# Optimization experiments

Measured on AMD Instinct MI355X. Metric: run time of the kernel, lower is better.

Reference implementation:

```python
import jax, jax.numpy as jnp
import numpy as np

B, C, N = 4, 256, 2048
H = 8
HD = C // H  # head_dim = 32


def setup_inputs() -> dict:
    key = jax.random.key(0)
    ks = jax.random.split(key, 5)
    s = 1.0 / np.sqrt(C)
    return {
        "x": jax.random.normal(ks[0], (B, C, 3, N), dtype=jnp.float32),
        "Wq": jax.random.normal(ks[1], (C, C), dtype=jnp.float32) * s,
        "Wk": jax.random.normal(ks[2], (C, C), dtype=jnp.float32) * s,
        "Wv": jax.random.normal(ks[3], (C, C), dtype=jnp.float32) * s,
        "Wo": jax.random.normal(ks[4], (C, C), dtype=jnp.float32) * s,
    }


def _vn_linear(W, x):
    # nn.Linear over channel axis: out[b,o,d,n] = sum_c W[o,c] x[b,c,d,n]
    return jnp.einsum('oc,bcdn->bodn', W, x)


def _heads(t):
    # [B,C,3,N] -> [B,H,N,HD,3]
    return t.reshape(B, H, HD, 3, N).transpose(0, 1, 4, 2, 3)


def reference(x, Wq, Wk, Wv, Wo):
    q = _heads(_vn_linear(Wq, x))
    k = _heads(_vn_linear(Wk, x))
    v = _heads(_vn_linear(Wv, x))
    # energy contracts over (head_dim, 3)
    energy = jnp.einsum('bhnci,bhmci->bhnm', q, k)
    attn = jax.nn.softmax(energy / np.sqrt(HD), axis=-1)
    out = jnp.einsum('bhnm,bhmci->bhnci', attn, v)
    # [B,H,N,HD,3] -> [B,C,3,N]
    out = out.transpose(0, 1, 3, 4, 2).reshape(B, C, 3, N)
    out = _vn_linear(Wo, out)
    return out + x
```

## Files before the change

kernel.cpp:

```cpp
#include <hip/hip_runtime.h>
#include <hip/hip_bf16.h>
#include <cmath>


typedef unsigned short u16;
typedef unsigned int   u32;
typedef u16   u16x8  __attribute__((ext_vector_type(8)));
typedef short s16x8  __attribute__((ext_vector_type(8)));
typedef float f32x4  __attribute__((ext_vector_type(4)));
typedef float f32x16 __attribute__((ext_vector_type(16)));

namespace {
constexpr int Nc = 2048, Fc = 96;
constexpr float SCALE_LOG2 = 0.17677669529663687f * 1.4426950408889634f;
constexpr float DEFER_THR  = 8.0f;
constexpr int KP = 104;
constexpr int VP = 72;
constexpr int VOFF = 64 * KP;
constexpr int SBUF = VOFF + 96 * VP;
}

__device__ inline float fast_exp2(float x) {
#if __has_builtin(__builtin_amdgcn_exp2f)
    return __builtin_amdgcn_exp2f(x);
#else
    return exp2f(x);
#endif
}

__device__ inline u16 f2bf(float x) {
    union { float f; unsigned u; } v; v.f = x;
    unsigned r = v.u + 0x7FFFu + ((v.u >> 16) & 1u);
    return (u16)(r >> 16);
}

__global__ __launch_bounds__(256) void wconv_kernel(
    const float* __restrict__ Wq, const float* __restrict__ Wk,
    const float* __restrict__ Wv, const float* __restrict__ Wo,
    u16* __restrict__ Wb)
{
    const int id = blockIdx.x * 256 + threadIdx.x;
    const int base = id * 8;
    const int o = base >> 8, c = base & 255;
    const int sel = o >> 8, ol = o & 255;
    const float* src = (sel == 0) ? Wq : (sel == 1) ? Wk : (sel == 2) ? Wv : Wo;
    const float sc = (sel == 0) ? SCALE_LOG2 : 1.0f;
    const float4 a = *(const float4*)&src[(size_t)ol * 256 + c];
    const float4 b = *(const float4*)&src[(size_t)ol * 256 + c + 4];
    u16x8 r;
    r[0]=f2bf(a.x*sc); r[1]=f2bf(a.y*sc); r[2]=f2bf(a.z*sc); r[3]=f2bf(a.w*sc);
    r[4]=f2bf(b.x*sc); r[5]=f2bf(b.y*sc); r[6]=f2bf(b.z*sc); r[7]=f2bf(b.w*sc);
    *(u16x8*)&Wb[(size_t)o * 256 + c] = r;
}

__global__ __launch_bounds__(256) void xt_kernel(
    const float* __restrict__ x, u16* __restrict__ xt)
{
    const int nt = blockIdx.x, ct = blockIdx.y, bi = blockIdx.z;
    const int b = bi / 3, i = bi % 3;
    const int t = (int)threadIdx.x;
    const int n0 = nt * 64, c0 = ct * 64;

    __shared__ u16 tile[64][72];

    const int n_l = t & 63;
#pragma unroll
    for (int it = 0; it < 16; ++it) {
        const int c_l = (t >> 6) + it * 4;
        tile[n_l][c_l] =
            f2bf(x[(((size_t)(b * 256 + c0 + c_l)) * 3 + i) * Nc + n0 + n_l]);
    }
    __syncthreads();
#pragma unroll
    for (int it = 0; it < 2; ++it) {
        const int idx = t + it * 256;
        const int nn = idx >> 3, part = idx & 7;
        *(u16x8*)&xt[((size_t)bi * Nc + n0 + nn) * 256 + c0 + part * 8] =
            *(const u16x8*)&tile[nn][part * 8];
    }
}

__global__ __launch_bounds__(256) void qkv_gemm_kernel(
    const u16* __restrict__ xt, const u16* __restrict__ wb,
    u16* __restrict__ Qt, u16* __restrict__ Kt, u16* __restrict__ Vf)
{
    const int nt = blockIdx.x;
    const int wy = blockIdx.y;
    const int bi = blockIdx.z;
    const int b = bi / 3, i = bi % 3;
    const int wsel = wy >> 1, ot = wy & 1;

    const u16* xs = xt + ((size_t)bi * Nc + nt * 128) * 256;
    const u16* ws = wb + (size_t)(wsel * 256 + ot * 128) * 256;

    __shared__ u16 xl[128][40];
    __shared__ u16 wl[128][40];

    const int t = (int)threadIdx.x;
    const int wv = t >> 6, lane = t & 63;
    const int g = lane >> 4, c16 = lane & 15;
    const int wr = wv >> 1, wc = wv & 1;

    f32x4 acc[4][4];
#pragma unroll
    for (int mi = 0; mi < 4; ++mi)
#pragma unroll
        for (int ni = 0; ni < 4; ++ni)
#pragma unroll
            for (int r = 0; r < 4; ++r) acc[mi][ni][r] = 0.f;

    for (int ks = 0; ks < 8; ++ks) {
        __syncthreads();
#pragma unroll
        for (int it = 0; it < 2; ++it) {
            const int idx = t + it * 256;
            const int row = idx >> 2, part = idx & 3;
            *(u16x8*)&xl[row][part * 8] =
                *(const u16x8*)&xs[(size_t)row * 256 + ks * 32 + part * 8];
            *(u16x8*)&wl[row][part * 8] =
                *(const u16x8*)&ws[(size_t)row * 256 + ks * 32 + part * 8];
        }
        __syncthreads();

        s16x8 af[4], bf[4];
        if (wsel < 2) {
#pragma unroll
            for (int mi = 0; mi < 4; ++mi) af[mi] = *(const s16x8*)&xl[wr*64 + mi*16 + c16][g*8];
#pragma unroll
            for (int ni = 0; ni < 4; ++ni) bf[ni] = *(const s16x8*)&wl[wc*64 + ni*16 + c16][g*8];
        } else {
#pragma unroll
            for (int mi = 0; mi < 4; ++mi) af[mi] = *(const s16x8*)&wl[wr*64 + mi*16 + c16][g*8];
#pragma unroll
            for (int ni = 0; ni < 4; ++ni) bf[ni] = *(const s16x8*)&xl[wc*64 + ni*16 + c16][g*8];
        }
#pragma unroll
        for (int mi = 0; mi < 4; ++mi)
#pragma unroll
            for (int ni = 0; ni < 4; ++ni)
                acc[mi][ni] = __builtin_amdgcn_mfma_f32_16x16x32_bf16(
                    af[mi], bf[ni], acc[mi][ni], 0, 0, 0);
    }

    if (wsel < 2) {
        u16* dst = wsel ? Kt : Qt;
#pragma unroll
        for (int mi = 0; mi < 4; ++mi)
#pragma unroll
            for (int ni = 0; ni < 4; ++ni) {
                const int o = ot * 128 + wc * 64 + ni * 16 + c16;
                const int h = o >> 5, cw = o & 31;
#pragma unroll
                for (int r = 0; r < 4; ++r) {
                    const int n = nt * 128 + wr * 64 + mi * 16 + g * 4 + r;
                    dst[((size_t)(b * 8 + h) * Nc + n) * Fc + i * 32 + cw] =
                        f2bf(acc[mi][ni][r]);
                }
            }
    } else {
#pragma unroll
        for (int mi = 0; mi < 4; ++mi)
#pragma unroll
            for (int ni = 0; ni < 4; ++ni) {
                const int n = nt * 128 + wc * 64 + ni * 16 + c16;
#pragma unroll
                for (int r = 0; r < 4; ++r) {
                    const int o = ot * 128 + wr * 64 + mi * 16 + g * 4 + r;
                    const int h = o >> 5, cw = o & 31;
                    Vf[((size_t)(b * 8 + h) * Fc + i * 32 + cw) * Nc + n] =
                        f2bf(acc[mi][ni][r]);
                }
            }
    }
}

__global__ __launch_bounds__(256) void attn_mfma_kernel(
    const u16* __restrict__ Qt, const u16* __restrict__ Kt,
    const u16* __restrict__ Vf, u16* __restrict__ aot)
{
    const int bid = (int)blockIdx.x;
    const int lid = (bid & 7) * 64 + (bid >> 3);
    const int bh = lid >> 4;
    const int qt = lid & 15;

    const int t    = (int)threadIdx.x;
    const int wq   = t >> 6;
    const int lane = t & 63;
    const int ql   = lane & 31;
    const int hi   = lane >> 5;

    __shared__ u16 sbuf[2][SBUF];

    const int qb = qt * 128 + wq * 32;

    s16x8 bq[6];
#pragma unroll
    for (int s6 = 0; s6 < 6; ++s6)
        bq[s6] = *(const s16x8*)&Qt[((size_t)bh * Nc + qb + ql) * Fc + s6 * 16 + hi * 8];

    const u16* g_src[6]; int g_str[6], g_dst[6];
#pragma unroll
    for (int it = 0; it < 6; ++it) {
        if (it < 3) {
            const int c = t + it * 256;
            const int row = c / 12, part = c - row * 12;
            g_src[it] = Kt + ((size_t)bh * Nc + row) * Fc + part * 8;
            g_str[it] = 64 * Fc;
            g_dst[it] = row * KP + part * 8;
        } else {
            const int c = t + (it - 3) * 256;
            const int f = c >> 3, part = c & 7;
            g_src[it] = Vf + ((size_t)bh * Fc + f) * Nc + part * 8;
            g_str[it] = 64;
            g_dst[it] = VOFF + f * VP + part * 8;
        }
    }

    f32x16 acc[3];
#pragma unroll
    for (int ft = 0; ft < 3; ++ft)
#pragma unroll
        for (int r = 0; r < 16; ++r) acc[ft][r] = 0.f;
    float m_s = -INFINITY, l_s = 0.f;

    u16x8 sreg[6];
#pragma unroll
    for (int it = 0; it < 6; ++it) sreg[it] = *(const u16x8*)g_src[it];
#pragma unroll
    for (int it = 0; it < 6; ++it) *(u16x8*)&sbuf[0][g_dst[it]] = sreg[it];
#pragma unroll
    for (int it = 0; it < 6; ++it)
        sreg[it] = *(const u16x8*)(g_src[it] + (size_t)g_str[it]);
    __syncthreads();

    for (int kt = 0; kt < 32; ++kt) {
        const int cur = kt & 1;
        if (kt < 31) {
#pragma unroll
            for (int it = 0; it < 6; ++it) *(u16x8*)&sbuf[cur ^ 1][g_dst[it]] = sreg[it];
        }
        if (kt < 30) {
#pragma unroll
            for (int it = 0; it < 6; ++it)
                sreg[it] = *(const u16x8*)(g_src[it] + (size_t)(kt + 2) * g_str[it]);
        }

        const u16* kb = &sbuf[cur][0];
        const u16* vb = &sbuf[cur][VOFF];

        f32x16 sv0, sv1;
#pragma unroll
        for (int r = 0; r < 16; ++r) { sv0[r] = 0.f; sv1[r] = 0.f; }
        __builtin_amdgcn_s_setprio(1);
#pragma unroll
        for (int s6 = 0; s6 < 6; ++s6) {
            const s16x8 ka0 = *(const s16x8*)&kb[ql * KP + s6 * 16 + hi * 8];
            sv0 = __builtin_amdgcn_mfma_f32_32x32x16_bf16(ka0, bq[s6], sv0, 0, 0, 0);
            const s16x8 ka1 = *(const s16x8*)&kb[(32 + ql) * KP + s6 * 16 + hi * 8];
            sv1 = __builtin_amdgcn_mfma_f32_32x32x16_bf16(ka1, bq[s6], sv1, 0, 0, 0);
        }
        __builtin_amdgcn_s_setprio(0);

        float mx[16];
#pragma unroll
        for (int r = 0; r < 16; ++r) mx[r] = fmaxf(sv0[r], sv1[r]);
#pragma unroll
        for (int s = 8; s > 0; s >>= 1)
#pragma unroll
            for (int r = 0; r < 16; ++r) if (r < s) mx[r] = fmaxf(mx[r], mx[r + s]);
        const float mloc = fmaxf(mx[0], __shfl_xor(mx[0], 32));

        if (__any(mloc > m_s + DEFER_THR)) {
            const float mnew = fmaxf(m_s, mloc);
            const float esc = fast_exp2(m_s - mnew);
            m_s = mnew; l_s *= esc;
#pragma unroll
            for (int ft = 0; ft < 3; ++ft)
#pragma unroll
                for (int r = 0; r < 16; ++r) acc[ft][r] *= esc;
        }

#pragma unroll
        for (int r = 0; r < 16; ++r) {
            sv0[r] = fast_exp2(sv0[r] - m_s);
            sv1[r] = fast_exp2(sv1[r] - m_s);
        }
        float ls[16];
#pragma unroll
        for (int r = 0; r < 16; ++r) ls[r] = sv0[r] + sv1[r];
#pragma unroll
        for (int s = 8; s > 0; s >>= 1)
#pragma unroll
            for (int r = 0; r < 16; ++r) if (r < s) ls[r] += ls[r + s];
        l_s += ls[0] + __shfl_xor(ls[0], 32);

        u32 pk0[8], pk1[8];
#pragma unroll
        for (int j = 0; j < 8; ++j) {
            asm("v_cvt_pk_bf16_f32 %0, %1, %2" : "=v"(pk0[j]) : "v"(sv0[2*j]), "v"(sv0[2*j+1]));
            asm("v_cvt_pk_bf16_f32 %0, %1, %2" : "=v"(pk1[j]) : "v"(sv1[2*j]), "v"(sv1[2*j+1]));
        }
        asm volatile("v_permlane32_swap_b32 %0, %1" : "+v"(pk0[0]), "+v"(pk0[2]));
        asm volatile("v_permlane32_swap_b32 %0, %1" : "+v"(pk0[1]), "+v"(pk0[3]));
        asm volatile("v_permlane32_swap_b32 %0, %1" : "+v"(pk0[4]), "+v"(pk0[6]));
        asm volatile("v_permlane32_swap_b32 %0, %1" : "+v"(pk0[5]), "+v"(pk0[7]));
        asm volatile("v_permlane32_swap_b32 %0, %1" : "+v"(pk1[0]), "+v"(pk1[2]));
        asm volatile("v_permlane32_swap_b32 %0, %1" : "+v"(pk1[1]), "+v"(pk1[3]));
        asm volatile("v_permlane32_swap_b32 %0, %1" : "+v"(pk1[4]), "+v"(pk1[6]));
        asm volatile("v_permlane32_swap_b32 %0, %1" : "+v"(pk1[5]), "+v"(pk1[7]));
        union U { u32 w[4]; s16x8 v; } pb[4];
        pb[0].w[0]=pk0[0]; pb[0].w[1]=pk0[1]; pb[0].w[2]=pk0[2]; pb[0].w[3]=pk0[3];
        pb[1].w[0]=pk0[4]; pb[1].w[1]=pk0[5]; pb[1].w[2]=pk0[6]; pb[1].w[3]=pk0[7];
        pb[2].w[0]=pk1[0]; pb[2].w[1]=pk1[1]; pb[2].w[2]=pk1[2]; pb[2].w[3]=pk1[3];
        pb[3].w[0]=pk1[4]; pb[3].w[1]=pk1[5]; pb[3].w[2]=pk1[6]; pb[3].w[3]=pk1[7];

        __builtin_amdgcn_s_setprio(1);
#pragma unroll
        for (int ft = 0; ft < 3; ++ft) {
#pragma unroll
            for (int ks = 0; ks < 4; ++ks) {
                const s16x8 va = *(const s16x8*)&vb[(ft * 32 + ql) * VP + ks * 16 + hi * 8];
                acc[ft] = __builtin_amdgcn_mfma_f32_32x32x16_bf16(va, pb[ks].v, acc[ft], 0, 0, 0);
            }
        }
        __builtin_amdgcn_s_setprio(0);

        __syncthreads();
    }

    const float inv = 1.f / l_s;
    u16* ot = &sbuf[0][0] + wq * (32 * 104);
#pragma unroll
    for (int ft = 0; ft < 3; ++ft)
#pragma unroll
        for (int r = 0; r < 16; ++r) {
            const int frow = (r & 3) + 8 * (r >> 2) + 4 * hi;
            ot[ql * 104 + ft * 32 + frow] = f2bf(acc[ft][r] * inv);
        }
    __syncthreads();

    u16x8 v6[6];
#pragma unroll
    for (int j = 0; j < 6; ++j)
        v6[j] = *(const u16x8*)&ot[ql * 104 + hi * 48 + j * 8];

    const int n = qb + ql;
    const int b_ = bh >> 3, h_ = bh & 7;
    const size_t base0 = ((size_t)(b_ * 3 + 0) * Nc + n) * 256 + h_ * 32;
    const size_t base1 = ((size_t)(b_ * 3 + 1) * Nc + n) * 256 + h_ * 32;
    const size_t base2 = ((size_t)(b_ * 3 + 2) * Nc + n) * 256 + h_ * 32;
    if (hi == 0) {
        *(u16x8*)&aot[base0 +  0] = v6[0];
        *(u16x8*)&aot[base0 +  8] = v6[1];
        *(u16x8*)&aot[base0 + 16] = v6[2];
        *(u16x8*)&aot[base0 + 24] = v6[3];
        *(u16x8*)&aot[base1 +  0] = v6[4];
        *(u16x8*)&aot[base1 +  8] = v6[5];
    } else {
        *(u16x8*)&aot[base1 + 16] = v6[0];
        *(u16x8*)&aot[base1 + 24] = v6[1];
        *(u16x8*)&aot[base2 +  0] = v6[2];
        *(u16x8*)&aot[base2 +  8] = v6[3];
        *(u16x8*)&aot[base2 + 16] = v6[4];
        *(u16x8*)&aot[base2 + 24] = v6[5];
    }
}

__global__ __launch_bounds__(256) void out_gemm_kernel(
    const u16* __restrict__ aot, const u16* __restrict__ wb,
    const float* __restrict__ x, float* __restrict__ out)
{
    const int nt = blockIdx.x, ot = blockIdx.y, bi = blockIdx.z;
    const int b = bi / 3, i = bi % 3;

    const u16* bs = aot + ((size_t)bi * Nc + nt * 128) * 256;
    const u16* ws = wb + (size_t)(768 + ot * 128) * 256;

    __shared__ u16 al[128][40];
    __shared__ u16 wl[128][40];

    const int t = (int)threadIdx.x;
    const int wv = t >> 6, lane = t & 63;
    const int g = lane >> 4, c16 = lane & 15;
    const int wr = wv >> 1, wc = wv & 1;

    f32x4 acc[4][4];
#pragma unroll
    for (int mi = 0; mi < 4; ++mi)
#pragma unroll
        for (int ni = 0; ni < 4; ++ni)
#pragma unroll
            for (int r = 0; r < 4; ++r) acc[mi][ni][r] = 0.f;

    for (int ks = 0; ks < 8; ++ks) {
        __syncthreads();
#pragma unroll
        for (int it = 0; it < 2; ++it) {
            const int idx = t + it * 256;
            const int row = idx >> 2, part = idx & 3;
            *(u16x8*)&al[row][part * 8] =
                *(const u16x8*)&bs[(size_t)row * 256 + ks * 32 + part * 8];
            *(u16x8*)&wl[row][part * 8] =
                *(const u16x8*)&ws[(size_t)row * 256 + ks * 32 + part * 8];
        }
        __syncthreads();

        s16x8 af[4], bf[4];
#pragma unroll
        for (int mi = 0; mi < 4; ++mi) af[mi] = *(const s16x8*)&wl[wr*64 + mi*16 + c16][g*8];
#pragma unroll
        for (int ni = 0; ni < 4; ++ni) bf[ni] = *(const s16x8*)&al[wc*64 + ni*16 + c16][g*8];
#pragma unroll
        for (int mi = 0; mi < 4; ++mi)
#pragma unroll
            for (int ni = 0; ni < 4; ++ni)
                acc[mi][ni] = __builtin_amdgcn_mfma_f32_16x16x32_bf16(
                    af[mi], bf[ni], acc[mi][ni], 0, 0, 0);
    }

#pragma unroll
    for (int mi = 0; mi < 4; ++mi)
#pragma unroll
        for (int ni = 0; ni < 4; ++ni) {
            const int n = nt * 128 + wc * 64 + ni * 16 + c16;
#pragma unroll
            for (int r = 0; r < 4; ++r) {
                const int o = ot * 128 + wr * 64 + mi * 16 + g * 4 + r;
                const size_t idx = ((size_t)(b * 256 + o) * 3 + i) * Nc + n;
                out[idx] = x[idx] + acc[mi][ni][r];
            }
        }
}

extern "C" void kernel_launch(void* const* d_in, const int* in_sizes, int n_in,
                              void* d_out, int out_size, void* d_ws, size_t ws_size,
                              hipStream_t stream) {
    const float* x  = (const float*)d_in[0];
    const float* Wq = (const float*)d_in[1];
    const float* Wk = (const float*)d_in[2];
    const float* Wv = (const float*)d_in[3];
    const float* Wo = (const float*)d_in[4];
    float* out = (float*)d_out;

    const size_t E = (size_t)32 * Fc * Nc;
    u16* xt  = (u16*)d_ws;
    u16* wbw = xt + E;
    u16* qt  = wbw + 262144;
    u16* kt  = qt + E;
    u16* vf  = kt + E;
    u16* aot = vf + E;

    dim3 blk(256);
    wconv_kernel    <<<dim3(128),        blk, 0, stream>>>(Wq, Wk, Wv, Wo, wbw);
    xt_kernel       <<<dim3(32, 4, 12),  blk, 0, stream>>>(x, xt);
    qkv_gemm_kernel <<<dim3(16, 6, 12),  blk, 0, stream>>>(xt, wbw, qt, kt, vf);
    attn_mfma_kernel<<<dim3(512),        blk, 0, stream>>>(qt, kt, vf, aot);
    out_gemm_kernel <<<dim3(16, 2, 12),  blk, 0, stream>>>(aot, wbw, x, out);
}
```

Before: 135.6 us.

## Software-pipeline QK^T one tile ahead with triple-buffered 32-key LDS tiles

Shrinks the attention key tile from 64 to 32 keys and triple-buffers K/V tiles in shared memory. The QK^T MFMAs for the next tile are issued before the softmax and PV of the current tile, with two score accumulators swapped alternately. The aim is to overlap the exp/reduction VALU work with matrix-core work and hide LDS loads. The cost is twice as many iterations and barriers, more LDS in use, and extra registers for the second score tile, and the setprio hints are removed.

```diff
diff --git a/kernel.cpp b/kernel.cpp
--- a/kernel.cpp
+++ b/kernel.cpp
@@ -15,8 +15,8 @@
 constexpr float SCALE_LOG2 = 0.17677669529663687f * 1.4426950408889634f;
 constexpr float DEFER_THR  = 8.0f;
 constexpr int KP = 104;
-constexpr int VP = 72;
-constexpr int VOFF = 64 * KP;
+constexpr int VP = 40;
+constexpr int VOFF = 32 * KP;
 constexpr int SBUF = VOFF + 96 * VP;
 }
 
@@ -183,13 +183,13 @@
     const int bh = lid >> 4;
     const int qt = lid & 15;
 
-    const int t    = (int)threadIdx.x;
-    const int wq   = t >> 6;
-    const int lane = t & 63;
+    const int t_   = (int)threadIdx.x;
+    const int wq   = t_ >> 6;
+    const int lane = t_ & 63;
     const int ql   = lane & 31;
     const int hi   = lane >> 5;
 
-    __shared__ u16 sbuf[2][SBUF];
+    __shared__ u16 sbuf[3 * SBUF];
 
     const int qb = qt * 128 + wq * 32;
 
@@ -198,20 +198,19 @@
     for (int s6 = 0; s6 < 6; ++s6)
         bq[s6] = *(const s16x8*)&Qt[((size_t)bh * Nc + qb + ql) * Fc + s6 * 16 + hi * 8];
 
-    const u16* g_src[6]; int g_str[6], g_dst[6];
-#pragma unroll
-    for (int it = 0; it < 6; ++it) {
-        if (it < 3) {
-            const int c = t + it * 256;
+    const u16* g_cur[3]; int g_str[3], g_dst[3];
+#pragma unroll
+    for (int it = 0; it < 3; ++it) {
+        const int c = t_ + it * 256;
+        if (c < 384) {
             const int row = c / 12, part = c - row * 12;
-            g_src[it] = Kt + ((size_t)bh * Nc + row) * Fc + part * 8;
-            g_str[it] = 64 * Fc;
+            g_cur[it] = Kt + ((size_t)bh * Nc + row) * Fc + part * 8;
+            g_str[it] = 32 * Fc;
             g_dst[it] = row * KP + part * 8;
         } else {
-            const int c = t + (it - 3) * 256;
-            const int f = c >> 3, part = c & 7;
-            g_src[it] = Vf + ((size_t)bh * Fc + f) * Nc + part * 8;
-            g_str[it] = 64;
+            const int c2 = c - 384, f = c2 >> 2, part = c2 & 3;
+            g_cur[it] = Vf + ((size_t)bh * Fc + f) * Nc + part * 8;
+            g_str[it] = 32;
             g_dst[it] = VOFF + f * VP + part * 8;
         }
     }
@@ -223,51 +222,61 @@
         for (int r = 0; r < 16; ++r) acc[ft][r] = 0.f;
     float m_s = -INFINITY, l_s = 0.f;
 
-    u16x8 sreg[6];
-#pragma unroll
-    for (int it = 0; it < 6; ++it) sreg[it] = *(const u16x8*)g_src[it];
-#pragma unroll
-    for (int it = 0; it < 6; ++it) *(u16x8*)&sbuf[0][g_dst[it]] = sreg[it];
-#pragma unroll
-    for (int it = 0; it < 6; ++it)
-        sreg[it] = *(const u16x8*)(g_src[it] + (size_t)g_str[it]);
+    u16* b0 = sbuf;
+    u16* b1 = sbuf + SBUF;
+    u16* b2 = sbuf + 2 * SBUF;
+
+    u16x8 sreg[3];
+#pragma unroll
+    for (int it = 0; it < 3; ++it) { sreg[it] = *(const u16x8*)g_cur[it]; g_cur[it] += g_str[it]; }
+#pragma unroll
+    for (int it = 0; it < 3; ++it) *(u16x8*)&b0[g_dst[it]] = sreg[it];
+#pragma unroll
+    for (int it = 0; it < 3; ++it) { sreg[it] = *(const u16x8*)g_cur[it]; g_cur[it] += g_str[it]; }
     __syncthreads();
 
-    for (int kt = 0; kt < 32; ++kt) {
-        const int cur = kt & 1;
-        if (kt < 31) {
-#pragma unroll
-            for (int it = 0; it < 6; ++it) *(u16x8*)&sbuf[cur ^ 1][g_dst[it]] = sreg[it];
-        }
-        if (kt < 30) {
-#pragma unroll
-            for (int it = 0; it < 6; ++it)
-                sreg[it] = *(const u16x8*)(g_src[it] + (size_t)(kt + 2) * g_str[it]);
-        }
-
-        const u16* kb = &sbuf[cur][0];
-        const u16* vb = &sbuf[cur][VOFF];
-
-        f32x16 sv0, sv1;
-#pragma unroll
-        for (int r = 0; r < 16; ++r) { sv0[r] = 0.f; sv1[r] = 0.f; }
-        __builtin_amdgcn_s_setprio(1);
-#pragma unroll
-        for (int s6 = 0; s6 < 6; ++s6) {
-            const s16x8 ka0 = *(const s16x8*)&kb[ql * KP + s6 * 16 + hi * 8];
-            sv0 = __builtin_amdgcn_mfma_f32_32x32x16_bf16(ka0, bq[s6], sv0, 0, 0, 0);
-            const s16x8 ka1 = *(const s16x8*)&kb[(32 + ql) * KP + s6 * 16 + hi * 8];
-            sv1 = __builtin_amdgcn_mfma_f32_32x32x16_bf16(ka1, bq[s6], sv1, 0, 0, 0);
-        }
-        __builtin_amdgcn_s_setprio(0);
-
-        float mx[16];
-#pragma unroll
-        for (int r = 0; r < 16; ++r) mx[r] = fmaxf(sv0[r], sv1[r]);
-#pragma unroll
-        for (int s = 8; s > 0; s >>= 1)
-#pragma unroll
-            for (int r = 0; r < 16; ++r) if (r < s) mx[r] = fmaxf(mx[r], mx[r + s]);
+    f32x16 svE, svO;
+#pragma unroll
+    for (int r = 0; r < 16; ++r) svE[r] = 0.f;
+#pragma unroll
+    for (int s6 = 0; s6 < 6; ++s6) {
+        const s16x8 ka = *(const s16x8*)&b0[ql * KP + s6 * 16 + hi * 8];
+        svE = __builtin_amdgcn_mfma_f32_32x32x16_bf16(ka, bq[s6], svE, 0, 0, 0);
+    }
+#pragma unroll
+    for (int it = 0; it < 3; ++it) *(u16x8*)&b1[g_dst[it]] = sreg[it];
+#pragma unroll
+    for (int it = 0; it < 3; ++it) { sreg[it] = *(const u16x8*)g_cur[it]; g_cur[it] += g_str[it]; }
+    __syncthreads();
+
+    u16 *bA = b0, *bB = b1, *bC = b2;
+
+    auto body = [&](int t, f32x16& SC, f32x16& SN) {
+        if (t < 63) {
+#pragma unroll
+            for (int r = 0; r < 16; ++r) SN[r] = 0.f;
+#pragma unroll
+            for (int s6 = 0; s6 < 6; ++s6) {
+                const s16x8 ka = *(const s16x8*)&bB[ql * KP + s6 * 16 + hi * 8];
+                SN = __builtin_amdgcn_mfma_f32_32x32x16_bf16(ka, bq[s6], SN, 0, 0, 0);
+            }
+        }
+        if (t < 62) {
+#pragma unroll
+            for (int it = 0; it < 3; ++it) *(u16x8*)&bC[g_dst[it]] = sreg[it];
+        }
+        if (t < 61) {
+#pragma unroll
+            for (int it = 0; it < 3; ++it) { sreg[it] = *(const u16x8*)g_cur[it]; g_cur[it] += g_str[it]; }
+        }
+
+        float mx[8];
+#pragma unroll
+        for (int r = 0; r < 8; ++r) mx[r] = fmaxf(SC[r], SC[r + 8]);
+#pragma unroll
+        for (int s = 4; s > 0; s >>= 1)
+#pragma unroll
+            for (int r = 0; r < 8; ++r) if (r < s) mx[r] = fmaxf(mx[r], mx[r + s]);
         const float mloc = fmaxf(mx[0], __shfl_xor(mx[0], 32));
 
         if (__any(mloc > m_s + DEFER_THR)) {
@@ -281,55 +290,49 @@
         }
 
 #pragma unroll
-        for (int r = 0; r < 16; ++r) {
-            sv0[r] = fast_exp2(sv0[r] - m_s);
-            sv1[r] = fast_exp2(sv1[r] - m_s);
-        }
-        float ls[16];
-#pragma unroll
-        for (int r = 0; r < 16; ++r) ls[r] = sv0[r] + sv1[r];
-#pragma unroll
-        for (int s = 8; s > 0; s >>= 1)
-#pragma unroll
-            for (int r = 0; r < 16; ++r) if (r < s) ls[r] += ls[r + s];
+        for (int r = 0; r < 16; ++r) SC[r] = fast_exp2(SC[r] - m_s);
+        float ls[8];
+#pragma unroll
+        for (int r = 0; r < 8; ++r) ls[r] = SC[r] + SC[r + 8];
+#pragma unroll
+        for (int s = 4; s > 0; s >>= 1)
+#pragma unroll
+            for (int r = 0; r < 8; ++r) if (r < s) ls[r] += ls[r + s];
         l_s += ls[0] + __shfl_xor(ls[0], 32);
 
-        u32 pk0[8], pk1[8];
-#pragma unroll
-        for (int j = 0; j < 8; ++j) {
-            asm("v_cvt_pk_bf16_f32 %0, %1, %2" : "=v"(pk0[j]) : "v"(sv0[2*j]), "v"(sv0[2*j+1]));
-            asm("v_cvt_pk_bf16_f32 %0, %1, %2" : "=v"(pk1[j]) : "v"(sv1[2*j]), "v"(sv1[2*j+1]));
-        }
-        asm volatile("v_permlane32_swap_b32 %0, %1" : "+v"(pk0[0]), "+v"(pk0[2]));
-        asm volatile("v_permlane32_swap_b32 %0, %1" : "+v"(pk0[1]), "+v"(pk0[3]));
-        asm volatile("v_permlane32_swap_b32 %0, %1" : "+v"(pk0[4]), "+v"(pk0[6]));
-        asm volatile("v_permlane32_swap_b32 %0, %1" : "+v"(pk0[5]), "+v"(pk0[7]));
-        asm volatile("v_permlane32_swap_b32 %0, %1" : "+v"(pk1[0]), "+v"(pk1[2]));
-        asm volatile("v_permlane32_swap_b32 %0, %1" : "+v"(pk1[1]), "+v"(pk1[3]));
-        asm volatile("v_permlane32_swap_b32 %0, %1" : "+v"(pk1[4]), "+v"(pk1[6]));
-        asm volatile("v_permlane32_swap_b32 %0, %1" : "+v"(pk1[5]), "+v"(pk1[7]));
-        union U { u32 w[4]; s16x8 v; } pb[4];
-        pb[0].w[0]=pk0[0]; pb[0].w[1]=pk0[1]; pb[0].w[2]=pk0[2]; pb[0].w[3]=pk0[3];
-        pb[1].w[0]=pk0[4]; pb[1].w[1]=pk0[5]; pb[1].w[2]=pk0[6]; pb[1].w[3]=pk0[7];
-        pb[2].w[0]=pk1[0]; pb[2].w[1]=pk1[1]; pb[2].w[2]=pk1[2]; pb[2].w[3]=pk1[3];
-        pb[3].w[0]=pk1[4]; pb[3].w[1]=pk1[5]; pb[3].w[2]=pk1[6]; pb[3].w[3]=pk1[7];
-
-        __builtin_amdgcn_s_setprio(1);
+        u32 pk8[8];
+#pragma unroll
+        for (int j = 0; j < 8; ++j)
+            asm("v_cvt_pk_bf16_f32 %0, %1, %2" : "=v"(pk8[j]) : "v"(SC[2*j]), "v"(SC[2*j+1]));
+        asm volatile("v_permlane32_swap_b32 %0, %1" : "+v"(pk8[0]), "+v"(pk8[2]));
+        asm volatile("v_permlane32_swap_b32 %0, %1" : "+v"(pk8[1]), "+v"(pk8[3]));
+        asm volatile("v_permlane32_swap_b32 %0, %1" : "+v"(pk8[4]), "+v"(pk8[6]));
+        asm volatile("v_permlane32_swap_b32 %0, %1" : "+v"(pk8[5]), "+v"(pk8[7]));
+        union U { u32 w[4]; s16x8 v; } pb0, pb1;
+        pb0.w[0]=pk8[0]; pb0.w[1]=pk8[1]; pb0.w[2]=pk8[2]; pb0.w[3]=pk8[3];
+        pb1.w[0]=pk8[4]; pb1.w[1]=pk8[5]; pb1.w[2]=pk8[6]; pb1.w[3]=pk8[7];
+
 #pragma unroll
         for (int ft = 0; ft < 3; ++ft) {
-#pragma unroll
-            for (int ks = 0; ks < 4; ++ks) {
-                const s16x8 va = *(const s16x8*)&vb[(ft * 32 + ql) * VP + ks * 16 + hi * 8];
-                acc[ft] = __builtin_amdgcn_mfma_f32_32x32x16_bf16(va, pb[ks].v, acc[ft], 0, 0, 0);
-            }
-        }
-        __builtin_amdgcn_s_setprio(0);
-
-        __syncthreads();
-    }
-
+            const s16x8 va0 = *(const s16x8*)&bA[VOFF + (ft * 32 + ql) * VP + hi * 8];
+            acc[ft] = __builtin_amdgcn_mfma_f32_32x32x16_bf16(va0, pb0.v, acc[ft], 0, 0, 0);
+            const s16x8 va1 = *(const s16x8*)&bA[VOFF + (ft * 32 + ql) * VP + 16 + hi * 8];
+            acc[ft] = __builtin_amdgcn_mfma_f32_32x32x16_bf16(va1, pb1.v, acc[ft], 0, 0, 0);
+        }
+
+        if (t < 63) __syncthreads();
+    };
+
+    for (int tb = 0; tb < 32; ++tb) {
+        body(2 * tb, svE, svO);
+        { u16* tmp = bA; bA = bB; bB = bC; bC = tmp; }
+        body(2 * tb + 1, svO, svE);
+        { u16* tmp = bA; bA = bB; bB = bC; bC = tmp; }
+    }
+
+    __syncthreads();
     const float inv = 1.f / l_s;
-    u16* ot = &sbuf[0][0] + wq * (32 * 104);
+    u16* ot = sbuf + wq * 3328;
 #pragma unroll
     for (int ft = 0; ft < 3; ++ft)
 #pragma unroll
```

Measured after the change: 132.0 us. 2.7% less time.
